# Kernel optimization log

Hardware: AMD Instinct MI355X
Metric: run time of the kernel (lower is better)

## Reference

```python
import jax, jax.numpy as jnp
import numpy as np

TEMPERATURE = 0.5  # sampler_config['temperature']
EPS = jnp.float32(np.finfo(np.float32).tiny)  # torch.finfo(float32).tiny


def setup_inputs() -> dict:
    key = jax.random.key(0)
    # att: [B graphs, N nodes per graph, M = Gnum_m subgraph samples]
    att = jax.random.normal(key, (256, 1024, 4), dtype=jnp.float32)
    return {"att": att, "k": 128}


def _continuous_topk(att, k, noise_key):
    """Iterative Gumbel-softmax relaxed top-k (Sampler.sample_subset +
    Sampler.continuous_topk with separate=False), batched over graphs (B)
    and subgraph samples (M).

    att: [B, N, M] node attention logits per graph per sample.
    Returns khot: [B, N, M], sum of k relaxed one-hot selections.
    """
    # gumbel_keys: z = -log(-log(U + eps))
    u = jax.random.uniform(noise_key, att.shape, dtype=att.dtype)
    att_g = att - jnp.log(-jnp.log(u + EPS))

    state0 = (att_g, jnp.zeros_like(att_g), jnp.zeros_like(att_g))

    def step(state, _):
        ag, onehot, khot = state
        khot_mask = jnp.maximum(1.0 - onehot, EPS)
        ag = ag + jnp.log(khot_mask)
        # softmax over the node axis (dim 0 of each per-graph slice in the original)
        onehot = jax.nn.softmax(ag / TEMPERATURE, axis=1)
        return (ag, onehot, khot + onehot), None

    (_, _, khot), _ = jax.lax.scan(step, state0, None, length=k)
    return khot


def reference(att, k):
    # Relaxed k-hot selection scores; the original then argsorts these per
    # graph to pick the top-k node indices (non-differentiable bookkeeping).
    return _continuous_topk(att, k, jax.random.key(42))
```

## Files before the change

kernel.cpp:

```cpp
#include <hip/hip_runtime.h>
#include <math.h>


#define N_NODES 1024

__device__ __forceinline__ unsigned rotl32(unsigned x, int r) {
  return (x << r) | (x >> (32 - r));
}

__device__ __forceinline__ void threefry2x32(unsigned k0, unsigned k1,
                                             unsigned& x0, unsigned& x1) {
  const unsigned ks0 = k0, ks1 = k1, ks2 = k0 ^ k1 ^ 0x1BD11BDAu;
  x0 += ks0; x1 += ks1;
  x0 += x1; x1 = rotl32(x1, 13); x1 ^= x0;
  x0 += x1; x1 = rotl32(x1, 15); x1 ^= x0;
  x0 += x1; x1 = rotl32(x1, 26); x1 ^= x0;
  x0 += x1; x1 = rotl32(x1, 6);  x1 ^= x0;
  x0 += ks1; x1 += ks2 + 1u;
  x0 += x1; x1 = rotl32(x1, 17); x1 ^= x0;
  x0 += x1; x1 = rotl32(x1, 29); x1 ^= x0;
  x0 += x1; x1 = rotl32(x1, 16); x1 ^= x0;
  x0 += x1; x1 = rotl32(x1, 24); x1 ^= x0;
  x0 += ks2; x1 += ks0 + 2u;
  x0 += x1; x1 = rotl32(x1, 13); x1 ^= x0;
  x0 += x1; x1 = rotl32(x1, 15); x1 ^= x0;
  x0 += x1; x1 = rotl32(x1, 26); x1 ^= x0;
  x0 += x1; x1 = rotl32(x1, 6);  x1 ^= x0;
  x0 += ks0; x1 += ks1 + 3u;
  x0 += x1; x1 = rotl32(x1, 17); x1 ^= x0;
  x0 += x1; x1 = rotl32(x1, 29); x1 ^= x0;
  x0 += x1; x1 = rotl32(x1, 16); x1 ^= x0;
  x0 += x1; x1 = rotl32(x1, 24); x1 ^= x0;
  x0 += ks1; x1 += ks2 + 4u;
  x0 += x1; x1 = rotl32(x1, 13); x1 ^= x0;
  x0 += x1; x1 = rotl32(x1, 15); x1 ^= x0;
  x0 += x1; x1 = rotl32(x1, 26); x1 ^= x0;
  x0 += x1; x1 = rotl32(x1, 6);  x1 ^= x0;
  x0 += ks2; x1 += ks0 + 5u;
}

template <int CTRL>
__device__ __forceinline__ float dpp_sum_step(float v) {
  int t = __builtin_amdgcn_update_dpp(0, __float_as_int(v), CTRL, 0xf, 0xf, true);
  return v + __int_as_float(t);
}
template <int CTRL>
__device__ __forceinline__ float dpp_max_step(float v) {
  int iv = __float_as_int(v);
  int t = __builtin_amdgcn_update_dpp(iv, iv, CTRL, 0xf, 0xf, false);
  return fmaxf(v, __int_as_float(t));
}

__device__ __forceinline__ float wave_sum64(float v) {
  v = dpp_sum_step<0x111>(v);
  v = dpp_sum_step<0x112>(v);
  v = dpp_sum_step<0x114>(v);
  v = dpp_sum_step<0x118>(v);
  v = dpp_sum_step<0x142>(v);
  v = dpp_sum_step<0x143>(v);
  return __int_as_float(__builtin_amdgcn_readlane(__float_as_int(v), 63));
}
__device__ __forceinline__ float wave_max64(float v) {
  v = dpp_max_step<0x111>(v);
  v = dpp_max_step<0x112>(v);
  v = dpp_max_step<0x114>(v);
  v = dpp_max_step<0x118>(v);
  v = dpp_max_step<0x142>(v);
  v = dpp_max_step<0x143>(v);
  return __int_as_float(__builtin_amdgcn_readlane(__float_as_int(v), 63));
}

__global__ __launch_bounds__(256)
void Sampler_72619307040792_kernel(const float* __restrict__ att,
                                   const int* __restrict__ kp,
                                   float* __restrict__ out) {
  const int b = blockIdx.x;
  const int tid = threadIdx.x;
  const int lane = tid & 63;
  const int m = tid >> 6;
  const int k = *kp;

  const float EPS = __uint_as_float(0x00800000u);
  const int base = b * 4096 + m;

  float w[16], kh[16], g[16];

#pragma unroll
  for (int j = 0; j < 16; ++j) {
    const int n = j * 64 + lane;
    const unsigned idx = (unsigned)(base + n * 4);
    unsigned c0 = 0u, c1 = idx;
    threefry2x32(0u, 42u, c0, c1);
    const unsigned bits = c0 ^ c1;
    const float u = __uint_as_float((bits >> 9) | 0x3F800000u) - 1.0f;
    const float gum = -logf(-logf(u + EPS));
    g[j] = 2.0f * (att[idx] + gum);
    kh[j] = 0.0f;
  }

  if (k <= 0) {
#pragma unroll
    for (int j = 0; j < 16; ++j) out[base + (j * 64 + lane) * 4] = 0.0f;
    return;
  }

  float mx = g[0];
#pragma unroll
  for (int j = 1; j < 16; ++j) mx = fmaxf(mx, g[j]);
  mx = wave_max64(mx);

  float sa[4] = {0.f, 0.f, 0.f, 0.f};
#pragma unroll
  for (int j = 0; j < 16; ++j) {
    w[j] = expf(g[j] - mx);
    sa[j & 3] += w[j];
  }
  float S = wave_sum64((sa[0] + sa[1]) + (sa[2] + sa[3]));
  float rinv = __builtin_amdgcn_rcpf(S);

  for (int it = 1; it < k; ++it) {
    float ta[4] = {0.f, 0.f, 0.f, 0.f};
#pragma unroll
    for (int j = 0; j < 16; ++j) {
      kh[j] = fmaf(w[j], rinv, kh[j]);
      float mk = fmaf(-w[j], rinv, 1.0f);
      mk = fmaxf(mk, EPS);
      const float wm = w[j] * mk;
      w[j] = wm * mk;
      ta[j & 3] += w[j];
    }
    S = wave_sum64((ta[0] + ta[1]) + (ta[2] + ta[3]));
    rinv = __builtin_amdgcn_rcpf(S);
  }

#pragma unroll
  for (int j = 0; j < 16; ++j) {
    kh[j] = fmaf(w[j], rinv, kh[j]);
    out[base + (j * 64 + lane) * 4] = kh[j];
  }
}

extern "C" void kernel_launch(void* const* d_in, const int* in_sizes, int n_in,
                              void* d_out, int out_size, void* d_ws, size_t ws_size,
                              hipStream_t stream) {
  const float* att = (const float*)d_in[0];
  const int* kp = (const int*)d_in[1];
  float* out = (float*)d_out;
  const int blocks = out_size / (N_NODES * 4);
  Sampler_72619307040792_kernel<<<blocks, 256, 0, stream>>>(att, kp, out);
}
```

Measured before the change: 36.61 us.

## Launch one wave per graph-sample column and shorten the iteration dependency chain

Each (graph, sample) column now runs in its own 64-thread block instead of four waves sharing a 256-thread block, giving the scheduler independent single-wave workgroups. The per-iteration update is rewritten: the clamp to EPS is dropped and w*(1-o)^2 is computed with two FMAs. The partial sums use a tree reduction, and the khot accumulation is moved after the sum so it overlaps the cross-lane reduction. Removing the EPS clamp changes numerics slightly when a one-hot value reaches 1.

```diff
diff --git a/kernel.cpp b/kernel.cpp
--- a/kernel.cpp
+++ b/kernel.cpp
@@ -70,14 +70,14 @@
   return __int_as_float(__builtin_amdgcn_readlane(__float_as_int(v), 63));
 }
 
-__global__ __launch_bounds__(256)
+__global__ __launch_bounds__(64, 1)
 void Sampler_72619307040792_kernel(const float* __restrict__ att,
                                    const int* __restrict__ kp,
                                    float* __restrict__ out) {
-  const int b = blockIdx.x;
-  const int tid = threadIdx.x;
-  const int lane = tid & 63;
-  const int m = tid >> 6;
+  const int col = blockIdx.x;
+  const int b = col >> 2;
+  const int m = col & 3;
+  const int lane = threadIdx.x;
   const int k = *kp;
 
   const float EPS = __uint_as_float(0x00800000u);
@@ -109,34 +109,41 @@
   for (int j = 1; j < 16; ++j) mx = fmaxf(mx, g[j]);
   mx = wave_max64(mx);
 
-  float sa[4] = {0.f, 0.f, 0.f, 0.f};
 #pragma unroll
-  for (int j = 0; j < 16; ++j) {
-    w[j] = expf(g[j] - mx);
-    sa[j & 3] += w[j];
-  }
-  float S = wave_sum64((sa[0] + sa[1]) + (sa[2] + sa[3]));
-  float rinv = __builtin_amdgcn_rcpf(S);
+  for (int j = 0; j < 16; ++j) w[j] = expf(g[j] - mx);
+  {
+    float t0 = (w[0] + w[1]) + (w[2] + w[3]);
+    float t1 = (w[4] + w[5]) + (w[6] + w[7]);
+    float t2 = (w[8] + w[9]) + (w[10] + w[11]);
+    float t3 = (w[12] + w[13]) + (w[14] + w[15]);
+    float S = wave_sum64((t0 + t1) + (t2 + t3));
+    float rinv = __builtin_amdgcn_rcpf(S);
 
-  for (int it = 1; it < k; ++it) {
-    float ta[4] = {0.f, 0.f, 0.f, 0.f};
+    for (int it = 1; it < k; ++it) {
+      float o[16];
+#pragma unroll
+      for (int j = 0; j < 16; ++j) o[j] = w[j] * rinv;
+#pragma unroll
+      for (int j = 0; j < 16; ++j) {
+        const float t = fmaf(-o[j], w[j], w[j]);
+        w[j] = fmaf(-o[j], t, t);
+      }
+      float s0 = (w[0] + w[1]) + (w[2] + w[3]);
+      float s1 = (w[4] + w[5]) + (w[6] + w[7]);
+      float s2 = (w[8] + w[9]) + (w[10] + w[11]);
+      float s3 = (w[12] + w[13]) + (w[14] + w[15]);
+      float sv = (s0 + s1) + (s2 + s3);
+#pragma unroll
+      for (int j = 0; j < 16; ++j) kh[j] += o[j];
+      S = wave_sum64(sv);
+      rinv = __builtin_amdgcn_rcpf(S);
+    }
+
 #pragma unroll
     for (int j = 0; j < 16; ++j) {
       kh[j] = fmaf(w[j], rinv, kh[j]);
-      float mk = fmaf(-w[j], rinv, 1.0f);
-      mk = fmaxf(mk, EPS);
-      const float wm = w[j] * mk;
-      w[j] = wm * mk;
-      ta[j & 3] += w[j];
+      out[base + (j * 64 + lane) * 4] = kh[j];
     }
-    S = wave_sum64((ta[0] + ta[1]) + (ta[2] + ta[3]));
-    rinv = __builtin_amdgcn_rcpf(S);
-  }
-
-#pragma unroll
-  for (int j = 0; j < 16; ++j) {
-    kh[j] = fmaf(w[j], rinv, kh[j]);
-    out[base + (j * 64 + lane) * 4] = kh[j];
   }
 }
 
@@ -146,6 +153,6 @@
   const float* att = (const float*)d_in[0];
   const int* kp = (const int*)d_in[1];
   float* out = (float*)d_out;
-  const int blocks = out_size / (N_NODES * 4);
-  Sampler_72619307040792_kernel<<<blocks, 256, 0, stream>>>(att, kp, out);
+  const int cols = out_size / N_NODES;
+  Sampler_72619307040792_kernel<<<cols, 64, 0, stream>>>(att, kp, out);
 }
```

New measurement: 31.78 us. 13.2% less time.
